# Optimization experiments

Measured on AMD Instinct MI355X. Metric: run time of the kernel, lower is better.

## Reference

```python
import jax, jax.numpy as jnp
import numpy as np

CUT_SIZE = 224  # cut_size init arg
CUTN = 32       # cutn init arg
CUT_POW = 1.0


def setup_inputs() -> dict:
    key = jax.random.key(0)
    B, C, H, W = 16, 3, 512, 512
    x = jax.random.normal(key, (B, C, H, W), dtype=jnp.float32)
    # Replicate the module's host-side RNG: size = rand()**cut_pow*(max-min)+min,
    # offset = randint(0, side - size + 1). Generated with numpy for determinism.
    rs = np.random.RandomState(0)
    max_size = min(H, W)
    min_size = min(H, W, CUT_SIZE)
    sizes = (rs.rand(CUTN) ** CUT_POW * (max_size - min_size) + min_size).astype(np.int32)
    offsetx = np.floor(rs.rand(CUTN) * (W - sizes + 1)).astype(np.int32)
    offsety = np.floor(rs.rand(CUTN) * (H - sizes + 1)).astype(np.int32)
    return {
        "x": x,
        "sizes": jnp.asarray(sizes),
        "offsetx": jnp.asarray(offsetx),
        "offsety": jnp.asarray(offsety),
    }


def reference(x, sizes, offsetx, offsety):
    # x: [B, C, H, W]; sizes/offsetx/offsety: [cutn] int32
    B, C, H, W = x.shape
    i = jnp.arange(CUT_SIZE, dtype=jnp.int32)
    # PyTorch F.interpolate default 'nearest': src = floor(out_idx * in/out)
    yidx = offsety[:, None] + (i[None, :] * sizes[:, None]) // CUT_SIZE  # [cutn, cut]
    xidx = offsetx[:, None] + (i[None, :] * sizes[:, None]) // CUT_SIZE  # [cutn, cut]
    # Fused crop + nearest-resize for all cutouts via one batched gather
    out = x[:, :, yidx[:, :, None], xidx[:, None, :]]  # [B, C, cutn, cut, cut]
    out = jnp.transpose(out, (2, 0, 1, 3, 4))           # [cutn, B, C, cut, cut]
    return out.reshape(CUTN * B, C, CUT_SIZE, CUT_SIZE)  # matches th.cat over cutn
```

## Files before the change

### kernel.cpp

```cpp
#include <hip/hip_runtime.h>


#define CUT_SIZE 224
#define CUTN     32
#define BATCH    16
#define CHAN     3
#define HEIGHT   512
#define WIDTH    512
#define R_SLICE  16
#define NSLICE   (HEIGHT / R_SLICE)
#define NIMG     (BATCH * CHAN)
#define WPB      4

typedef const __attribute__((address_space(1))) void* gas_ptr;
typedef __attribute__((address_space(3))) void*       las_ptr;

__device__ __forceinline__ void stage_row(const float* src_row, float* lds_buf, int lane)
{
    __builtin_amdgcn_global_load_lds((gas_ptr)(src_row + lane * 4),
                                     (las_ptr)(lds_buf), 16, 0, 0);
    __builtin_amdgcn_global_load_lds((gas_ptr)(src_row + 256 + lane * 4),
                                     (las_ptr)(lds_buf + 256), 16, 0, 0);
}

__global__ __launch_bounds__(256) void make_cutouts_kernel(
    const float* __restrict__ x,
    const int*   __restrict__ sizes,
    const int*   __restrict__ offsetx,
    const int*   __restrict__ offsety,
    float*       __restrict__ out)
{
    __shared__ __align__(16) float lds[R_SLICE][WIDTH];

    const int wid  = threadIdx.x >> 6;
    const int lane = threadIdx.x & 63;

    const int bid   = blockIdx.x;
    const int img   = bid >> 5;
    const int slice = bid & (NSLICE - 1);
    const int b     = img / CHAN;
    const int c     = img % CHAN;
    const int y0    = slice * R_SLICE;

    const float* img_p = x + (size_t)img * (HEIGHT * WIDTH);

    #pragma unroll
    for (int r = 0; r < R_SLICE / WPB; ++r) {
        const int row = wid * (R_SLICE / WPB) + r;
        stage_row(img_p + (size_t)(y0 + row) * WIDTH, &lds[row][0], lane);
    }
    asm volatile("s_waitcnt vmcnt(0)" ::: "memory");
    __syncthreads();

    for (int nn = 0; nn < CUTN / WPB; ++nn) {
        const int n  = wid + nn * WPB;
        const int sz = sizes[n];
        const int ox = offsetx[n];
        const int oy = offsety[n];

        const int d0 = y0 - oy;
        const int d1 = y0 + R_SLICE - oy;
        int i0 = (d0 <= 0) ? 0 : (int)(((unsigned)(d0 * CUT_SIZE) + (unsigned)sz - 1u) / (unsigned)sz);
        int i1 = (d1 <= 0) ? 0 : (int)(((unsigned)(d1 * CUT_SIZE) + (unsigned)sz - 1u) / (unsigned)sz);
        if (i1 > CUT_SIZE) i1 = CUT_SIZE;
        if (i0 >= i1) continue;

        const unsigned usz = (unsigned)sz;
        const int xi0 = ox + (int)(((unsigned)(lane      ) * usz) / CUT_SIZE);
        const int xi1 = ox + (int)(((unsigned)(lane +  64) * usz) / CUT_SIZE);
        const int xi2 = ox + (int)(((unsigned)(lane + 128) * usz) / CUT_SIZE);
        const int xi3 = (lane < 32)
                      ? ox + (int)(((unsigned)(lane + 192) * usz) / CUT_SIZE)
                      : xi0;

        float* og = out + (size_t)((n * BATCH + b) * CHAN + c) * (CUT_SIZE * CUT_SIZE);

        for (int i = i0; i < i1; ++i) {
            const int y = oy + (int)(((unsigned)(i * (int)usz)) / CUT_SIZE);
            const float* lrow = &lds[y - y0][0];

            const float v0 = lrow[xi0];
            const float v1 = lrow[xi1];
            const float v2 = lrow[xi2];
            const float v3 = lrow[xi3];

            float* orow = og + (size_t)i * CUT_SIZE;
            orow[lane      ] = v0;
            orow[lane +  64] = v1;
            orow[lane + 128] = v2;
            if (lane < 32) orow[lane + 192] = v3;
        }
    }
}

extern "C" void kernel_launch(void* const* d_in, const int* in_sizes, int n_in,
                              void* d_out, int out_size, void* d_ws, size_t ws_size,
                              hipStream_t stream) {
    const float* x       = (const float*)d_in[0];
    const int*   sizes   = (const int*)d_in[1];
    const int*   offsetx = (const int*)d_in[2];
    const int*   offsety = (const int*)d_in[3];
    float*       out     = (float*)d_out;

    const int grid = NIMG * NSLICE;
    make_cutouts_kernel<<<grid, 256, 0, stream>>>(x, sizes, offsetx, offsety, out);
}
```

Before: 352.5 us.

## Replace static slice blocks with atomic per-row work queue across partitions

Drops the fixed grid of 16-row slices per image. Each wave now pulls single-row tasks from one of eight atomic counters in workspace, stages that row into its own LDS buffer, and writes every cutout row that maps to it. The goal is to balance load dynamically, since slices hit very different numbers of cutouts, and to remove block-wide barriers. In exchange it adds an atomic per row, a memset launch, and per-row scans over all 32 cutouts with integer divisions.

Result: slower. 379.8 us (+7.8%).

```diff
diff --git a/kernel.cpp b/kernel.cpp
--- a/kernel.cpp
+++ b/kernel.cpp
@@ -7,10 +7,11 @@
 #define CHAN     3
 #define HEIGHT   512
 #define WIDTH    512
-#define R_SLICE  16
-#define NSLICE   (HEIGHT / R_SLICE)
 #define NIMG     (BATCH * CHAN)
 #define WPB      4
+#define NPART    8
+#define IMG_PER_PART   (NIMG / NPART)
+#define TASKS_PER_PART (IMG_PER_PART * HEIGHT)
 
 typedef const __attribute__((address_space(1))) void* gas_ptr;
 typedef __attribute__((address_space(3))) void*       las_ptr;
@@ -28,68 +29,69 @@
     const int*   __restrict__ sizes,
     const int*   __restrict__ offsetx,
     const int*   __restrict__ offsety,
-    float*       __restrict__ out)
+    float*       __restrict__ out,
+    int*         __restrict__ counters)
 {
-    __shared__ __align__(16) float lds[R_SLICE][WIDTH];
+    __shared__ __align__(16) float lds[WPB][WIDTH];
 
     const int wid  = threadIdx.x >> 6;
     const int lane = threadIdx.x & 63;
 
-    const int bid   = blockIdx.x;
-    const int img   = bid >> 5;
-    const int slice = bid & (NSLICE - 1);
-    const int b     = img / CHAN;
-    const int c     = img % CHAN;
-    const int y0    = slice * R_SLICE;
+    const int p   = blockIdx.x & (NPART - 1);
+    int* ctr = counters + p * 32;
 
-    const float* img_p = x + (size_t)img * (HEIGHT * WIDTH);
+    float* myl = &lds[wid][0];
 
-    #pragma unroll
-    for (int r = 0; r < R_SLICE / WPB; ++r) {
-        const int row = wid * (R_SLICE / WPB) + r;
-        stage_row(img_p + (size_t)(y0 + row) * WIDTH, &lds[row][0], lane);
-    }
-    asm volatile("s_waitcnt vmcnt(0)" ::: "memory");
-    __syncthreads();
+    for (;;) {
+        int t;
+        if (lane == 0) t = atomicAdd(ctr, 1);
+        t = __builtin_amdgcn_readfirstlane(t);
+        if (t >= TASKS_PER_PART) break;
 
-    for (int nn = 0; nn < CUTN / WPB; ++nn) {
-        const int n  = wid + nn * WPB;
-        const int sz = sizes[n];
-        const int ox = offsetx[n];
-        const int oy = offsety[n];
+        const int img = p * IMG_PER_PART + (t >> 9);
+        const int y   = t & (HEIGHT - 1);
 
-        const int d0 = y0 - oy;
-        const int d1 = y0 + R_SLICE - oy;
-        int i0 = (d0 <= 0) ? 0 : (int)(((unsigned)(d0 * CUT_SIZE) + (unsigned)sz - 1u) / (unsigned)sz);
-        int i1 = (d1 <= 0) ? 0 : (int)(((unsigned)(d1 * CUT_SIZE) + (unsigned)sz - 1u) / (unsigned)sz);
-        if (i1 > CUT_SIZE) i1 = CUT_SIZE;
-        if (i0 >= i1) continue;
+        stage_row(x + ((size_t)img * HEIGHT + y) * WIDTH, myl, lane);
+        asm volatile("s_waitcnt vmcnt(0)" ::: "memory");
+        __builtin_amdgcn_sched_barrier(0);
 
-        const unsigned usz = (unsigned)sz;
-        const int xi0 = ox + (int)(((unsigned)(lane      ) * usz) / CUT_SIZE);
-        const int xi1 = ox + (int)(((unsigned)(lane +  64) * usz) / CUT_SIZE);
-        const int xi2 = ox + (int)(((unsigned)(lane + 128) * usz) / CUT_SIZE);
-        const int xi3 = (lane < 32)
-                      ? ox + (int)(((unsigned)(lane + 192) * usz) / CUT_SIZE)
-                      : xi0;
+        const int b = img / CHAN;
+        const int c = img % CHAN;
 
-        float* og = out + (size_t)((n * BATCH + b) * CHAN + c) * (CUT_SIZE * CUT_SIZE);
+        for (int n = 0; n < CUTN; ++n) {
+            const int      sz  = sizes[n];
+            const unsigned usz = (unsigned)sz;
+            const unsigned ud  = (unsigned)(y - offsety[n]);
+            if (ud >= usz) continue;
 
-        for (int i = i0; i < i1; ++i) {
-            const int y = oy + (int)(((unsigned)(i * (int)usz)) / CUT_SIZE);
-            const float* lrow = &lds[y - y0][0];
+            unsigned i = (ud * 224u + usz - 1u) / usz;
+            if (i >= 224u) continue;
+            if ((i * usz) / 224u != ud) continue;
 
-            const float v0 = lrow[xi0];
-            const float v1 = lrow[xi1];
-            const float v2 = lrow[xi2];
-            const float v3 = lrow[xi3];
+            const int ox  = offsetx[n];
+            const int xi0 = ox + (int)(((unsigned)(lane      ) * usz) / 224u);
+            const int xi1 = ox + (int)(((unsigned)(lane +  64) * usz) / 224u);
+            const int xi2 = ox + (int)(((unsigned)(lane + 128) * usz) / 224u);
+            const int xi3 = (lane < 32)
+                          ? ox + (int)(((unsigned)(lane + 192) * usz) / 224u)
+                          : xi0;
 
-            float* orow = og + (size_t)i * CUT_SIZE;
+            const float v0 = myl[xi0];
+            const float v1 = myl[xi1];
+            const float v2 = myl[xi2];
+            const float v3 = myl[xi3];
+
+            float* orow = out + (size_t)((n * BATCH + b) * CHAN + c)
+                                  * (CUT_SIZE * CUT_SIZE)
+                              + (size_t)i * CUT_SIZE;
             orow[lane      ] = v0;
             orow[lane +  64] = v1;
             orow[lane + 128] = v2;
             if (lane < 32) orow[lane + 192] = v3;
         }
+
+        asm volatile("s_waitcnt lgkmcnt(0)" ::: "memory");
+        __builtin_amdgcn_sched_barrier(0);
     }
 }
 
@@ -101,7 +103,11 @@
     const int*   offsetx = (const int*)d_in[2];
     const int*   offsety = (const int*)d_in[3];
     float*       out     = (float*)d_out;
+    int*         counters = (int*)d_ws;
 
-    const int grid = NIMG * NSLICE;
-    make_cutouts_kernel<<<grid, 256, 0, stream>>>(x, sizes, offsetx, offsety, out);
+    hipMemsetAsync(d_ws, 0, NPART * 32 * sizeof(int), stream);
+
+    const int grid = 2048;
+    make_cutouts_kernel<<<grid, 256, 0, stream>>>(x, sizes, offsetx, offsety,
+                                                  out, counters);
 }
```
